# Kernel optimization log

Measured on AMD Instinct MI355X. Metric: run time of the kernel, lower is better.

Reference implementation:

```python
import jax, jax.numpy as jnp
import numpy as np

B, T, E, H, D = 2, 2048, 1024, 16, 64
SCALE = 1.0 / float(np.sqrt(D))


def setup_inputs() -> dict:
    key = jax.random.key(0)
    ks = jax.random.split(key, 8)
    n = lambda k, sh, s=1.0: jax.random.normal(k, sh, dtype=jnp.float32) * s
    # torch nn.Linear weights are [out_features, in_features]; xavier-ish scale
    return {
        "query": n(ks[0], (B, T, E)),
        "key_": n(ks[1], (B, T, E)),
        "value": n(ks[2], (B, T, E)),
        "attn_mask": n(ks[3], (T, T), 0.1),
        "Wq": n(ks[4], (H * D, E), 1.0 / float(np.sqrt(E))),
        "Wk": n(ks[5], (H * D, E), 1.0 / float(np.sqrt(E))),
        "Wv": n(ks[6], (H * D, E), 1.0 / float(np.sqrt(E))),
        "Wo": n(ks[7], (E, H * D), 1.0 / float(np.sqrt(H * D))),
    }


def reference(query, key_, value, attn_mask, Wq, Wk, Wv, Wo):
    # projections (no bias), reshape to [B, T, H, D]
    Q = (query @ Wq.T).reshape(B, T, H, D)
    K = (key_ @ Wk.T).reshape(B, -1, H, D)
    V = (value @ Wv.T).reshape(B, -1, H, D)
    # scores [B, T, H, S]; additive [T, S] mask broadcast over B and H
    score = jnp.einsum("bthd,bshd->bths", Q, K) * SCALE
    score = score + attn_mask[:, None, :]
    prob = jax.nn.softmax(score, axis=-1)  # dropout is identity in eval mode
    attn = jnp.einsum("bths,bshd->bthd", prob, V)  # [B, T, H, D]
    x = attn.reshape(B, T, H * D) @ Wo.T  # output projection
    return x
```

## Files before the change

### kernel.cpp

```cpp
#include <hip/hip_runtime.h>


typedef __attribute__((ext_vector_type(8))) short s8v;
typedef __attribute__((ext_vector_type(4))) float f4v;

typedef __attribute__((address_space(1))) const void* gas_t;
typedef __attribute__((address_space(3))) void* las_t;

#define GLOAD_LDS(src, dst) \
  __builtin_amdgcn_global_load_lds((gas_t)(src), (las_t)(dst), 16, 0, 0)
#define MFMA16(a, b, c) __builtin_amdgcn_mfma_f32_16x16x32_bf16((a), (b), (c), 0, 0, 0)

static constexpr int Bn = 2, Tn = 2048, En = 1024, Hn = 16, Dn = 64;
static constexpr float kScale = 0.125f;
static constexpr float kLog2e = 1.4426950408889634f;

union P8 { s8v v; unsigned short u[8]; };

__device__ __forceinline__ unsigned short f2bf(float f) {
  unsigned int x = __float_as_uint(f);
  x += 0x7fffu + ((x >> 16) & 1u);
  return (unsigned short)(x >> 16);
}

__device__ __forceinline__ int cvtpk(float lo, float hi) {
  int r;
  asm("v_cvt_pk_bf16_f32 %0, %1, %2" : "=v"(r) : "v"(lo), "v"(hi));
  return r;
}

__device__ __forceinline__ void cast8(const float* __restrict__ src, int j,
                                      unsigned short* __restrict__ out, int i) {
  float4 a = ((const float4*)src)[2 * j];
  float4 b = ((const float4*)src)[2 * j + 1];
  P8 p;
  p.u[0] = f2bf(a.x); p.u[1] = f2bf(a.y); p.u[2] = f2bf(a.z); p.u[3] = f2bf(a.w);
  p.u[4] = f2bf(b.x); p.u[5] = f2bf(b.y); p.u[6] = f2bf(b.z); p.u[7] = f2bf(b.w);
  ((s8v*)out)[i] = p.v;
}

__global__ void cast3_kernel(const float* __restrict__ a, const float* __restrict__ b,
                             const float* __restrict__ c,
                             unsigned short* __restrict__ out, int n8) {
  int i = blockIdx.x * blockDim.x + threadIdx.x;
  const int stride = gridDim.x * blockDim.x;
  const int total = 3 * n8;
  for (; i < total; i += stride) {
    const float* src = (i < n8) ? a : (i < 2 * n8) ? b : c;
    const int j = (i < n8) ? i : (i < 2 * n8) ? i - n8 : i - 2 * n8;
    cast8(src, j, out, i);
  }
}

__global__ void cast4_kernel(const float* __restrict__ a, const float* __restrict__ b,
                             const float* __restrict__ c, const float* __restrict__ d,
                             unsigned short* __restrict__ out, int n8) {
  int i = blockIdx.x * blockDim.x + threadIdx.x;
  const int stride = gridDim.x * blockDim.x;
  const int total = 4 * n8;
  for (; i < total; i += stride) {
    const int which = i / n8;
    const float* src = (which == 0) ? a : (which == 1) ? b : (which == 2) ? c : d;
    cast8(src, i - which * n8, out, i);
  }
}

__global__ __launch_bounds__(64) void maskpack_kernel(const float* __restrict__ mask,
                                                      float* __restrict__ mP) {
  __shared__ float tile[16][65];
  const int qt = blockIdx.x, st = blockIdx.y;
  const int tid = threadIdx.x;
#pragma unroll
  for (int i = 0; i < 16; ++i)
    tile[i][tid] = mask[(size_t)(qt * 16 + i) * Tn + st * 64 + tid];
  __syncthreads();
  const int lr = tid & 15, lg = tid >> 4;
  float o[16];
#pragma unroll
  for (int n = 0; n < 4; ++n)
#pragma unroll
    for (int rg = 0; rg < 4; ++rg)
      o[n * 4 + rg] = tile[lr][n * 16 + lg * 4 + rg] * kLog2e;
  float4* dst = (float4*)(mP + ((size_t)(qt * 32 + st) * 64 + tid) * 16);
#pragma unroll
  for (int q4 = 0; q4 < 4; ++q4)
    dst[q4] = make_float4(o[q4 * 4], o[q4 * 4 + 1], o[q4 * 4 + 2], o[q4 * 4 + 3]);
}

template <int MODE>
__global__ __launch_bounds__(256) void gemm_bt(const unsigned short* __restrict__ A,
                                               const unsigned short* __restrict__ W,
                                               void* __restrict__ Cout, float scale) {
  constexpr int N = 1024, K = 1024;
  __shared__ unsigned short As[2][128 * 64];
  __shared__ unsigned short Bs[2][128 * 64];
  const int tid = threadIdx.x;
  const int w = tid >> 6, l = tid & 63;
  const int wr = w >> 1, wc = w & 1;
  const int lr = l & 15, lg = l >> 4;

  const int gx = gridDim.x;
  int id = blockIdx.y * gx + blockIdx.x;
  id = (id & 7) * 32 + (id >> 3);
  const int m0 = (id / gx) * 128, n0 = (id % gx) * 128;

  auto stage = [&](int k0, int buf) {
#pragma unroll
    for (int jj = 0; jj < 4; ++jj) {
      const int q = jj * 256 + tid;
      const int r = q >> 3, c = q & 7;
      const int cs = c ^ (r & 7);
      GLOAD_LDS(A + (size_t)(m0 + r) * K + k0 + cs * 8,
                (char*)As[buf] + (jj * 256 + w * 64) * 16);
      GLOAD_LDS(W + (size_t)(n0 + r) * K + k0 + cs * 8,
                (char*)Bs[buf] + (jj * 256 + w * 64) * 16);
    }
  };

  stage(0, 0);
  __syncthreads();

  f4v acc[4][4] = {};

  for (int k0 = 0, t = 0; k0 < K; k0 += 64, ++t) {
    const int cur = t & 1;
    if (k0 + 64 < K) stage(k0 + 64, cur ^ 1);
#pragma unroll
    for (int kk = 0; kk < 2; ++kk) {
      s8v af[4], bf[4];
      const int kc = kk * 4 + lg;
#pragma unroll
      for (int i = 0; i < 4; ++i) {
        const int ra = wr * 64 + i * 16 + lr;
        const int rb = wc * 64 + i * 16 + lr;
        af[i] = *(const s8v*)((const char*)As[cur] + ra * 128 + ((kc ^ (ra & 7)) << 4));
        bf[i] = *(const s8v*)((const char*)Bs[cur] + rb * 128 + ((kc ^ (rb & 7)) << 4));
      }
#pragma unroll
      for (int mi = 0; mi < 4; ++mi)
#pragma unroll
        for (int nj = 0; nj < 4; ++nj)
          acc[mi][nj] = MFMA16(af[mi], bf[nj], acc[mi][nj]);
    }
    __syncthreads();
  }

#pragma unroll
  for (int mi = 0; mi < 4; ++mi)
#pragma unroll
    for (int nj = 0; nj < 4; ++nj)
#pragma unroll
      for (int rg = 0; rg < 4; ++rg) {
        const int row = m0 + wr * 64 + mi * 16 + lg * 4 + rg;
        const int col = n0 + wc * 64 + nj * 16 + lr;
        const float v = acc[mi][nj][rg];
        if (MODE == 0) {
          ((float*)Cout)[(size_t)row * N + col] = v;
        } else if (MODE == 1) {
          const int b = row >> 11, t = row & (Tn - 1);
          const int hh = col >> 6, d = col & 63;
          ((unsigned short*)Cout)[(((size_t)(b * Hn + hh) * Tn + t) << 6) + d] =
              f2bf(v * scale);
        } else {
          const int hh = row >> 6, d = row & 63;
          const int b = col >> 11, t = col & (Tn - 1);
          ((unsigned short*)Cout)[((size_t)(b * Hn + hh) * 64 + d) * Tn + t] =
              f2bf(v);
        }
      }
}

__global__ __launch_bounds__(256, 4) void attn_kernel(
    const unsigned short* __restrict__ Q,
    const unsigned short* __restrict__ Kg,
    const unsigned short* __restrict__ Vt,
    const float* __restrict__ maskP,
    unsigned short* __restrict__ Out) {
  __shared__ unsigned short Ks[2][64 * 64];
  __shared__ unsigned short Vs[2][64 * 64];

  const int tid = threadIdx.x;
  const int w = tid >> 6, lane = tid & 63;
  const int lr = lane & 15, lg = lane >> 4;
  const int qt = blockIdx.x, h = blockIdx.y, b = blockIdx.z;
  const size_t hoff = (size_t)(b * Hn + h) * Tn * Dn;
  const unsigned short* Qh = Q + hoff;
  const unsigned short* Kh = Kg + hoff;
  const unsigned short* Vh = Vt + hoff;
  const int qw = qt * 64 + w * 16;
  const float* mP = maskP + (size_t)(qt * 4 + w) * 32 * 1024 + lane * 16;

  auto stage = [&](int s0, int buf) {
#pragma unroll
    for (int jj = 0; jj < 2; ++jj) {
      const int cq = jj * 256 + tid;
      const int r = cq >> 3, cc = cq & 7;
      const int cs = cc ^ (r & 7);
      GLOAD_LDS(Kh + (size_t)(s0 + r) * 64 + cs * 8,
                (char*)Ks[buf] + (jj * 256 + w * 64) * 16);
      GLOAD_LDS(Vh + (size_t)r * Tn + s0 + cs * 8,
                (char*)Vs[buf] + (jj * 256 + w * 64) * 16);
    }
  };

  s8v qf[2];
#pragma unroll
  for (int kk = 0; kk < 2; ++kk)
    qf[kk] = *(const s8v*)(Qh + (size_t)(qw + lr) * 64 + kk * 32 + lg * 8);

  float lsum = 0.f;
  f4v oacc[4] = {};

  const int srcA = lr + ((lg & 1) << 5);
  const int srcB = srcA + 16;
  const int hi = lg >> 1;

  stage(0, 0);
  __syncthreads();

  for (int s0 = 0, t = 0; s0 < Tn; s0 += 64, ++t, mP += 1024) {
    const int cur = t & 1;
    if (s0 + 64 < Tn) stage(s0 + 64, cur ^ 1);

    f4v scT[4];
#pragma unroll
    for (int n = 0; n < 4; ++n) scT[n] = *(const f4v*)(mP + n * 4);

#pragma unroll
    for (int kk = 0; kk < 2; ++kk) {
#pragma unroll
      for (int n = 0; n < 4; ++n) {
        const int row = n * 16 + lr;
        s8v kf = *(const s8v*)((const char*)Ks[cur] + row * 128 +
                               (((kk * 4 + lg) ^ (lr & 7)) << 4));
        scT[n] = MFMA16(kf, qf[kk], scT[n]);
      }
    }

    float ssum = 0.f;
#pragma unroll
    for (int n = 0; n < 4; ++n)
#pragma unroll
      for (int rg = 0; rg < 4; ++rg) {
        const float p = exp2f(scT[n][rg]);
        scT[n][rg] = p;
        ssum += p;
      }
    ssum += __shfl_xor(ssum, 16);
    ssum += __shfl_xor(ssum, 32);
    lsum += ssum;

    int pw0[4], pw1[4];
#pragma unroll
    for (int n = 0; n < 4; ++n) {
      pw0[n] = cvtpk(scT[n][0], scT[n][1]);
      pw1[n] = cvtpk(scT[n][2], scT[n][3]);
    }

#pragma unroll
    for (int kk = 0; kk < 2; ++kk) {
      const int a0 = __shfl(pw0[2 * kk], srcA), b0 = __shfl(pw0[2 * kk + 1], srcA);
      const int a1 = __shfl(pw1[2 * kk], srcA), b1 = __shfl(pw1[2 * kk + 1], srcA);
      const int a2 = __shfl(pw0[2 * kk], srcB), b2 = __shfl(pw0[2 * kk + 1], srcB);
      const int a3 = __shfl(pw1[2 * kk], srcB), b3 = __shfl(pw1[2 * kk + 1], srcB);
      union { s8v v; int x[4]; } pf;
      pf.x[0] = hi ? b0 : a0;
      pf.x[1] = hi ? b1 : a1;
      pf.x[2] = hi ? b2 : a2;
      pf.x[3] = hi ? b3 : a3;
#pragma unroll
      for (int n = 0; n < 4; ++n) {
        const int rd = n * 16 + lr;
        s8v vf = *(const s8v*)((const char*)Vs[cur] + rd * 128 +
                               (((kk * 4 + lg) ^ (lr & 7)) << 4));
        oacc[n] = MFMA16(pf.v, vf, oacc[n]);
      }
    }
    __syncthreads();
  }

#pragma unroll
  for (int rg = 0; rg < 4; ++rg) {
    const float inv = 1.f / __shfl(lsum, lg * 4 + rg);
    const int t = qw + lg * 4 + rg;
#pragma unroll
    for (int n = 0; n < 4; ++n) {
      const int d = n * 16 + lr;
      Out[((size_t)(b * Tn + t) * Hn + h) * 64 + d] = f2bf(oacc[n][rg] * inv);
    }
  }
}

extern "C" void kernel_launch(void* const* d_in, const int* in_sizes, int n_in,
                              void* d_out, int out_size, void* d_ws, size_t ws_size,
                              hipStream_t stream) {
  (void)in_sizes; (void)n_in; (void)out_size; (void)ws_size;
  const float* query = (const float*)d_in[0];
  const float* key_  = (const float*)d_in[1];
  const float* value = (const float*)d_in[2];
  const float* mask  = (const float*)d_in[3];
  const float* Wq    = (const float*)d_in[4];
  const float* Wk    = (const float*)d_in[5];
  const float* Wv    = (const float*)d_in[6];
  const float* Wo    = (const float*)d_in[7];
  float* out = (float*)d_out;

  char* ws = (char*)d_ws;
  const size_t MB = 1024 * 1024;
  unsigned short* qx  = (unsigned short*)(ws + 0 * MB);
  unsigned short* vx  = (unsigned short*)(ws + 16 * MB);
  unsigned short* Qh  = (unsigned short*)(ws + 24 * MB);
  unsigned short* Kh  = (unsigned short*)(ws + 32 * MB);
  unsigned short* Vtg = (unsigned short*)(ws + 40 * MB);
  unsigned short* atb = (unsigned short*)(ws + 48 * MB);
  unsigned short* wqx = (unsigned short*)(ws + 56 * MB);
  unsigned short* wkx = (unsigned short*)(ws + 58 * MB);
  unsigned short* wvx = (unsigned short*)(ws + 60 * MB);
  unsigned short* wox = (unsigned short*)(ws + 62 * MB);
  float* maskP = (float*)(ws + 0 * MB);

  const int nBig = Bn * Tn * En / 8;
  const int nW   = En * En / 8;
  cast3_kernel<<<2048, 256, 0, stream>>>(query, key_, value, qx, nBig);
  cast4_kernel<<<1024, 256, 0, stream>>>(Wq, Wk, Wv, Wo, wqx, nW);

  dim3 gg(1024 / 128, 4096 / 128);
  gemm_bt<1><<<gg, 256, 0, stream>>>(qx, wqx, Qh, kScale * kLog2e);
  gemm_bt<1><<<gg, 256, 0, stream>>>(qx + 8 * MB / 2, wkx, Kh, 1.0f);
  gemm_bt<2><<<dim3(4096 / 128, 1024 / 128), 256, 0, stream>>>(wvx, vx, Vtg, 1.0f);

  maskpack_kernel<<<dim3(128, 32), 64, 0, stream>>>(mask, maskP);

  attn_kernel<<<dim3(Tn / 64, Hn, Bn), 256, 0, stream>>>(Qh, Kh, Vtg, maskP, atb);

  gemm_bt<0><<<gg, 256, 0, stream>>>(atb, wox, out, 1.0f);
}
```

Measured before the change: 195.0 us.

## Merge QKV projections into one launch, pack mask as bf16, load K from registers

The three projection GEMMs are merged into one 768-block launch that picks Q, K or V work per block, using single-buffered LDS tiles. The pre-scaled mask is stored as packed bf16 instead of fp32, which halves mask traffic in the attention kernel at the cost of mask precision. K fragments are now read directly from global memory into registers instead of being staged through LDS. Attention blocks are remapped so that all blocks for a given head land on the same XCD for L2 reuse, and exp2f is replaced with the hardware exp2 builtin.

```diff
diff --git a/kernel.cpp b/kernel.cpp
--- a/kernel.cpp
+++ b/kernel.cpp
@@ -10,6 +10,12 @@
 #define GLOAD_LDS(src, dst) \
   __builtin_amdgcn_global_load_lds((gas_t)(src), (las_t)(dst), 16, 0, 0)
 #define MFMA16(a, b, c) __builtin_amdgcn_mfma_f32_16x16x32_bf16((a), (b), (c), 0, 0, 0)
+
+#if __has_builtin(__builtin_amdgcn_exp2f)
+#define EXP2(x) __builtin_amdgcn_exp2f(x)
+#else
+#define EXP2(x) exp2f(x)
+#endif
 
 static constexpr int Bn = 2, Tn = 2048, En = 1024, Hn = 16, Dn = 64;
 static constexpr float kScale = 0.125f;
@@ -66,7 +72,7 @@
 }
 
 __global__ __launch_bounds__(64) void maskpack_kernel(const float* __restrict__ mask,
-                                                      float* __restrict__ mP) {
+                                                      unsigned int* __restrict__ mPB) {
   __shared__ float tile[16][65];
   const int qt = blockIdx.x, st = blockIdx.y;
   const int tid = threadIdx.x;
@@ -81,16 +87,99 @@
 #pragma unroll
     for (int rg = 0; rg < 4; ++rg)
       o[n * 4 + rg] = tile[lr][n * 16 + lg * 4 + rg] * kLog2e;
-  float4* dst = (float4*)(mP + ((size_t)(qt * 32 + st) * 64 + tid) * 16);
-#pragma unroll
-  for (int q4 = 0; q4 < 4; ++q4)
-    dst[q4] = make_float4(o[q4 * 4], o[q4 * 4 + 1], o[q4 * 4 + 2], o[q4 * 4 + 3]);
-}
-
-template <int MODE>
-__global__ __launch_bounds__(256) void gemm_bt(const unsigned short* __restrict__ A,
-                                               const unsigned short* __restrict__ W,
-                                               void* __restrict__ Cout, float scale) {
+  unsigned int wds[8];
+#pragma unroll
+  for (int i = 0; i < 8; ++i)
+    wds[i] = ((unsigned int)f2bf(o[2 * i + 1]) << 16) | f2bf(o[2 * i]);
+  uint4* dst = (uint4*)(mPB + ((size_t)(qt * 32 + st) * 64 + tid) * 8);
+  dst[0] = make_uint4(wds[0], wds[1], wds[2], wds[3]);
+  dst[1] = make_uint4(wds[4], wds[5], wds[6], wds[7]);
+}
+
+__global__ __launch_bounds__(256) void gemm3_kernel(
+    const unsigned short* __restrict__ qx, const unsigned short* __restrict__ kx,
+    const unsigned short* __restrict__ vxa, const unsigned short* __restrict__ wqx,
+    const unsigned short* __restrict__ wkx, const unsigned short* __restrict__ wvx,
+    unsigned short* __restrict__ Qh, unsigned short* __restrict__ Kh,
+    unsigned short* __restrict__ Vtg) {
+  constexpr int K = 1024;
+  __shared__ unsigned short As[128 * 64];
+  __shared__ unsigned short Bs[128 * 64];
+  const int tid = threadIdx.x;
+  const int w = tid >> 6, l = tid & 63;
+  const int wr = w >> 1, wc = w & 1;
+  const int lr = l & 15, lg = l >> 4;
+
+  const int id0 = blockIdx.x;
+  const int rid = (id0 & 7) * 96 + (id0 >> 3);
+  const int z = rid >> 8;
+  const int t8 = rid & 255;
+  const int m0 = (z < 2) ? (t8 >> 3) * 128 : (t8 & 7) * 128;
+  const int n0 = (z < 2) ? (t8 & 7) * 128 : (t8 >> 3) * 128;
+
+  const unsigned short* A = (z == 0) ? qx : (z == 1) ? kx : wvx;
+  const unsigned short* W = (z == 0) ? wqx : (z == 1) ? wkx : vxa;
+
+  f4v acc[4][4] = {};
+
+  for (int k0 = 0; k0 < K; k0 += 64) {
+#pragma unroll
+    for (int jj = 0; jj < 4; ++jj) {
+      const int q = jj * 256 + tid;
+      const int r = q >> 3, c = q & 7;
+      const int cs = c ^ (r & 7);
+      GLOAD_LDS(A + (size_t)(m0 + r) * K + k0 + cs * 8,
+                (char*)As + (jj * 256 + w * 64) * 16);
+      GLOAD_LDS(W + (size_t)(n0 + r) * K + k0 + cs * 8,
+                (char*)Bs + (jj * 256 + w * 64) * 16);
+    }
+    __syncthreads();
+#pragma unroll
+    for (int kk = 0; kk < 2; ++kk) {
+      s8v af[4], bf[4];
+      const int kc = kk * 4 + lg;
+#pragma unroll
+      for (int i = 0; i < 4; ++i) {
+        const int ra = wr * 64 + i * 16 + lr;
+        const int rb = wc * 64 + i * 16 + lr;
+        af[i] = *(const s8v*)((const char*)As + ra * 128 + ((kc ^ (ra & 7)) << 4));
+        bf[i] = *(const s8v*)((const char*)Bs + rb * 128 + ((kc ^ (rb & 7)) << 4));
+      }
+#pragma unroll
+      for (int mi = 0; mi < 4; ++mi)
+#pragma unroll
+        for (int nj = 0; nj < 4; ++nj)
+          acc[mi][nj] = MFMA16(af[mi], bf[nj], acc[mi][nj]);
+    }
+    __syncthreads();
+  }
+
+  const float scale = (z == 0) ? kScale * kLog2e : 1.0f;
+#pragma unroll
+  for (int mi = 0; mi < 4; ++mi)
+#pragma unroll
+    for (int nj = 0; nj < 4; ++nj)
+#pragma unroll
+      for (int rg = 0; rg < 4; ++rg) {
+        const int row = m0 + wr * 64 + mi * 16 + lg * 4 + rg;
+        const int col = n0 + wc * 64 + nj * 16 + lr;
+        const float v = acc[mi][nj][rg];
+        if (z < 2) {
+          const int b = row >> 11, t = row & (Tn - 1);
+          const int hh = col >> 6, d = col & 63;
+          unsigned short* o = (z == 0) ? Qh : Kh;
+          o[(((size_t)(b * Hn + hh) * Tn + t) << 6) + d] = f2bf(v * scale);
+        } else {
+          const int hh = row >> 6, d = row & 63;
+          const int b = col >> 11, t = col & (Tn - 1);
+          Vtg[((size_t)(b * Hn + hh) * 64 + d) * Tn + t] = f2bf(v);
+        }
+      }
+}
+
+__global__ __launch_bounds__(256) void gemm_out(const unsigned short* __restrict__ A,
+                                                const unsigned short* __restrict__ W,
+                                                float* __restrict__ Cout) {
   constexpr int N = 1024, K = 1024;
   __shared__ unsigned short As[2][128 * 64];
   __shared__ unsigned short Bs[2][128 * 64];
@@ -153,20 +242,7 @@
       for (int rg = 0; rg < 4; ++rg) {
         const int row = m0 + wr * 64 + mi * 16 + lg * 4 + rg;
         const int col = n0 + wc * 64 + nj * 16 + lr;
-        const float v = acc[mi][nj][rg];
-        if (MODE == 0) {
-          ((float*)Cout)[(size_t)row * N + col] = v;
-        } else if (MODE == 1) {
-          const int b = row >> 11, t = row & (Tn - 1);
-          const int hh = col >> 6, d = col & 63;
-          ((unsigned short*)Cout)[(((size_t)(b * Hn + hh) * Tn + t) << 6) + d] =
-              f2bf(v * scale);
-        } else {
-          const int hh = row >> 6, d = row & 63;
-          const int b = col >> 11, t = col & (Tn - 1);
-          ((unsigned short*)Cout)[((size_t)(b * Hn + hh) * 64 + d) * Tn + t] =
-              f2bf(v);
-        }
+        Cout[(size_t)row * N + col] = acc[mi][nj][rg];
       }
 }
 
@@ -174,30 +250,34 @@
     const unsigned short* __restrict__ Q,
     const unsigned short* __restrict__ Kg,
     const unsigned short* __restrict__ Vt,
-    const float* __restrict__ maskP,
+    const unsigned int* __restrict__ mPB,
     unsigned short* __restrict__ Out) {
-  __shared__ unsigned short Ks[2][64 * 64];
   __shared__ unsigned short Vs[2][64 * 64];
 
   const int tid = threadIdx.x;
   const int w = tid >> 6, lane = tid & 63;
   const int lr = lane & 15, lg = lane >> 4;
-  const int qt = blockIdx.x, h = blockIdx.y, b = blockIdx.z;
-  const size_t hoff = (size_t)(b * Hn + h) * Tn * Dn;
+
+  const int lin = blockIdx.x;
+  const int xcd = lin & 7, slot = lin >> 3;
+  const int bh = xcd * 4 + (slot >> 5);
+  const int qtB = slot & 31;
+  const int b = bh >> 4, h = bh & 15;
+
+  const size_t hoff = (size_t)bh * Tn * Dn;
   const unsigned short* Qh = Q + hoff;
   const unsigned short* Kh = Kg + hoff;
   const unsigned short* Vh = Vt + hoff;
-  const int qw = qt * 64 + w * 16;
-  const float* mP = maskP + (size_t)(qt * 4 + w) * 32 * 1024 + lane * 16;
-
-  auto stage = [&](int s0, int buf) {
+  const int qw = qtB * 64 + w * 16;
+  const unsigned int* mp = mPB + ((size_t)(qtB * 4 + w) * 32 * 64 + lane) * 8;
+  const unsigned short* Kp = Kh + lr * 64 + lg * 8;
+
+  auto stageV = [&](int s0, int buf) {
 #pragma unroll
     for (int jj = 0; jj < 2; ++jj) {
       const int cq = jj * 256 + tid;
       const int r = cq >> 3, cc = cq & 7;
       const int cs = cc ^ (r & 7);
-      GLOAD_LDS(Kh + (size_t)(s0 + r) * 64 + cs * 8,
-                (char*)Ks[buf] + (jj * 256 + w * 64) * 16);
       GLOAD_LDS(Vh + (size_t)r * Tn + s0 + cs * 8,
                 (char*)Vs[buf] + (jj * 256 + w * 64) * 16);
     }
@@ -215,34 +295,44 @@
   const int srcB = srcA + 16;
   const int hi = lg >> 1;
 
-  stage(0, 0);
+  stageV(0, 0);
   __syncthreads();
 
-  for (int s0 = 0, t = 0; s0 < Tn; s0 += 64, ++t, mP += 1024) {
+  for (int s0 = 0, t = 0; s0 < Tn; s0 += 64, ++t, mp += 512) {
     const int cur = t & 1;
-    if (s0 + 64 < Tn) stage(s0 + 64, cur ^ 1);
-
+    if (s0 + 64 < Tn) stageV(s0 + 64, cur ^ 1);
+
+    s8v kf[2][4];
+#pragma unroll
+    for (int kk = 0; kk < 2; ++kk)
+#pragma unroll
+      for (int n = 0; n < 4; ++n)
+        kf[kk][n] = *(const s8v*)(Kp + (size_t)(s0 + n * 16) * 64 + kk * 32);
+
+    const uint4 u0 = *(const uint4*)(mp);
+    const uint4 u1 = *(const uint4*)(mp + 4);
+    const unsigned int wd[8] = {u0.x, u0.y, u0.z, u0.w, u1.x, u1.y, u1.z, u1.w};
     f4v scT[4];
 #pragma unroll
-    for (int n = 0; n < 4; ++n) scT[n] = *(const f4v*)(mP + n * 4);
-
-#pragma unroll
-    for (int kk = 0; kk < 2; ++kk) {
-#pragma unroll
-      for (int n = 0; n < 4; ++n) {
-        const int row = n * 16 + lr;
-        s8v kf = *(const s8v*)((const char*)Ks[cur] + row * 128 +
-                               (((kk * 4 + lg) ^ (lr & 7)) << 4));
-        scT[n] = MFMA16(kf, qf[kk], scT[n]);
-      }
-    }
+    for (int n = 0; n < 4; ++n) {
+      scT[n][0] = __uint_as_float(wd[2 * n] << 16);
+      scT[n][1] = __uint_as_float(wd[2 * n] & 0xffff0000u);
+      scT[n][2] = __uint_as_float(wd[2 * n + 1] << 16);
+      scT[n][3] = __uint_as_float(wd[2 * n + 1] & 0xffff0000u);
+    }
+
+#pragma unroll
+    for (int kk = 0; kk < 2; ++kk)
+#pragma unroll
+      for (int n = 0; n < 4; ++n)
+        scT[n] = MFMA16(kf[kk][n], qf[kk], scT[n]);
 
     float ssum = 0.f;
 #pragma unroll
     for (int n = 0; n < 4; ++n)
 #pragma unroll
       for (int rg = 0; rg < 4; ++rg) {
-        const float p = exp2f(scT[n][rg]);
+        const float p = EXP2(scT[n][rg]);
         scT[n][rg] = p;
         ssum += p;
       }
@@ -308,6 +398,7 @@
   char* ws = (char*)d_ws;
   const size_t MB = 1024 * 1024;
   unsigned short* qx  = (unsigned short*)(ws + 0 * MB);
+  unsigned short* kx  = (unsigned short*)(ws + 8 * MB);
   unsigned short* vx  = (unsigned short*)(ws + 16 * MB);
   unsigned short* Qh  = (unsigned short*)(ws + 24 * MB);
   unsigned short* Kh  = (unsigned short*)(ws + 32 * MB);
@@ -317,21 +408,18 @@
   unsigned short* wkx = (unsigned short*)(ws + 58 * MB);
   unsigned short* wvx = (unsigned short*)(ws + 60 * MB);
   unsigned short* wox = (unsigned short*)(ws + 62 * MB);
-  float* maskP = (float*)(ws + 0 * MB);
+  unsigned int* mPB = (unsigned int*)(ws + 0 * MB);
 
   const int nBig = Bn * Tn * En / 8;
   const int nW   = En * En / 8;
   cast3_kernel<<<2048, 256, 0, stream>>>(query, key_, value, qx, nBig);
   cast4_kernel<<<1024, 256, 0, stream>>>(Wq, Wk, Wv, Wo, wqx, nW);
 
-  dim3 gg(1024 / 128, 4096 / 128);
-  gemm_bt<1><<<gg, 256, 0, stream>>>(qx, wqx, Qh, kScale * kLog2e);
-  gemm_bt<1><<<gg, 256, 0, stream>>>(qx + 8 * MB / 2, wkx, Kh, 1.0f);
-  gemm_bt<2><<<dim3(4096 / 128, 1024 / 128), 256, 0, stream>>>(wvx, vx, Vtg, 1.0f);
-
-  maskpack_kernel<<<dim3(128, 32), 64, 0, stream>>>(mask, maskP);
-
-  attn_kernel<<<dim3(Tn / 64, Hn, Bn), 256, 0, stream>>>(Qh, Kh, Vtg, maskP, atb);
-
-  gemm_bt<0><<<gg, 256, 0, stream>>>(atb, wox, out, 1.0f);
-}
+  gemm3_kernel<<<768, 256, 0, stream>>>(qx, kx, vx, wqx, wkx, wvx, Qh, Kh, Vtg);
+
+  maskpack_kernel<<<dim3(128, 32), 64, 0, stream>>>(mask, mPB);
+
+  attn_kernel<<<1024, 256, 0, stream>>>(Qh, Kh, Vtg, mPB, atb);
+
+  gemm_out<<<dim3(8, 32), 256, 0, stream>>>(atb, wox, out);
+}
```

Result: slower. 228.0 us (+16.9%).
